# Performance work log

Hardware: AMD Instinct MI355X
Metric: run time of the kernel (lower is better)

## Reference

```python
import jax, jax.numpy as jnp
import numpy as np
from functools import partial

N = 10000      # nodes
E = 100000     # edges
WIDTH = 64     # node hidden width
KER_W = 1024   # kernel MLP hidden width
KER_IN = 6     # edge feature dim
DEPTH = 6


def setup_inputs() -> dict:
    key = jax.random.key(0)
    ks = jax.random.split(key, 16)

    def glorot(k, shape):
        fan_in = shape[0]
        return jax.random.normal(k, shape, dtype=jnp.float32) / np.sqrt(fan_in)

    inp = {
        "x": jax.random.normal(ks[0], (N, 1), dtype=jnp.float32),
        "edge_index": jax.random.randint(ks[1], (2, E), 0, N, dtype=jnp.int32),
        "edge_attr": jax.random.uniform(ks[2], (E, KER_IN), dtype=jnp.float32),
        # fc1: in_width=1 -> width
        "fc1_w": glorot(ks[3], (1, WIDTH)),
        "fc1_b": jnp.zeros((WIDTH,), jnp.float32),
        # kernel DenseNet: ker_in -> ker_width -> ker_width -> width**2 (ReLU between)
        "k1_w": glorot(ks[4], (KER_IN, KER_W)),
        "k1_b": jnp.zeros((KER_W,), jnp.float32),
        "k2_w": glorot(ks[5], (KER_W, KER_W)),
        "k2_b": jnp.zeros((KER_W,), jnp.float32),
        "k3_w": glorot(ks[6], (KER_W, WIDTH * WIDTH)),
        "k3_b": jnp.zeros((WIDTH * WIDTH,), jnp.float32),
        # NNConv_old root weight + bias
        "root_w": glorot(ks[7], (WIDTH, WIDTH)),
        "conv_b": jnp.zeros((WIDTH,), jnp.float32),
        # fc2: width -> 1
        "fc2_w": glorot(ks[8], (WIDTH, 1)),
        "fc2_b": jnp.zeros((1,), jnp.float32),
    }
    return inp


def reference(x, edge_index, edge_attr, fc1_w, fc1_b, k1_w, k1_b, k2_w, k2_b,
              k3_w, k3_b, root_w, conv_b, fc2_w, fc2_b):
    src = edge_index[0]  # x_j (source, gathered)
    dst = edge_index[1]  # aggregation target

    # Per-edge kernel MLP -> [E, width, width]. edge_attr is constant across
    # depth iterations, so compute the edge weights once (same math).
    h = jax.nn.relu(edge_attr @ k1_w + k1_b)
    h = jax.nn.relu(h @ k2_w + k2_b)
    ew = (h @ k3_w + k3_b).reshape(E, WIDTH, WIDTH)

    # mean aggregation denominators (scatter_mean semantics: deg clamped to 1)
    deg = jax.ops.segment_sum(jnp.ones((E,), jnp.float32), dst, num_segments=N)
    deg = jnp.maximum(deg, 1.0)[:, None]  # [N,1]

    z = x @ fc1_w + fc1_b  # [N, width]
    for _ in range(DEPTH):
        msg = jnp.einsum('ei,eio->eo', z[src], ew)            # gather + per-edge matmul
        agg = jax.ops.segment_sum(msg, dst, num_segments=N)   # scatter-add
        agg = agg / deg                                       # mean
        z = jax.nn.relu(agg + z @ root_w + conv_b)
    return z @ fc2_w + fc2_b  # [N, 1]
```

## Files before the change

kernel.cpp:

```cpp
#include <hip/hip_runtime.h>
#include <hip/hip_bf16.h>

#define N_NODES 10000
#define N_EDGES 100000
#define DEPTH   6
#define E_CHUNK 12500

typedef __attribute__((ext_vector_type(8))) short short8;
typedef __attribute__((ext_vector_type(4))) float f32x4;
typedef unsigned short u16;

__device__ __forceinline__ float bf2f(u16 u) {
    union { float f; unsigned int i; } v; v.i = ((unsigned int)u) << 16; return v.f;
}
__device__ __forceinline__ u16 f2bf(float f) {
    union { float f; unsigned int i; } v; v.f = f;
    unsigned int x = v.i;
    unsigned int r = (x + 0x7fffu + ((x >> 16) & 1u)) >> 16;
    return (u16)r;
}

__device__ __forceinline__ void gload_lds16(const void* g, void* s) {
    __builtin_amdgcn_global_load_lds((const __attribute__((address_space(1))) void*)g,
                                     (__attribute__((address_space(3))) void*)s, 16, 0, 0);
}

__global__ void k2_transpose_kernel(const float* __restrict__ k2w, u16* __restrict__ k2T) {
    int idx = blockIdx.x * 256 + threadIdx.x;
    int n = idx >> 10, k = idx & 1023;
    k2T[idx] = f2bf(k2w[k * 1024 + n]);
}
__global__ void k3_permT_kernel(const float* __restrict__ k3w, u16* __restrict__ k3pT) {
    int idx = blockIdx.x * 256 + threadIdx.x;
    int n = idx >> 10, c = idx & 1023;
    k3pT[idx] = f2bf(k3w[(size_t)c * 4096 + (n & 63) * 64 + (n >> 6)]);
}
__global__ void b3_permute_kernel(const float* __restrict__ b3, float* __restrict__ b3p) {
    int n = blockIdx.x * 256 + threadIdx.x;
    if (n >= 4096) return;
    b3p[n] = b3[(n & 63) * 64 + (n >> 6)];
}

__global__ void deg_kernel(const int* __restrict__ ei, float* __restrict__ deg) {
    int e = blockIdx.x * 256 + threadIdx.x;
    if (e < N_EDGES) atomicAdd(&deg[ei[N_EDGES + e]], 1.0f);
}

__global__ void gemm1_kernel(const float* __restrict__ ea, const float* __restrict__ k1w,
                             const float* __restrict__ k1b, u16* __restrict__ h1, int e0) {
    int idx = blockIdx.x * 256 + threadIdx.x;
    int c = idx & 1023;
    int e = (idx >> 10) + e0;
    float acc = k1b[c];
#pragma unroll
    for (int i = 0; i < 6; i++) acc += ea[e * 6 + i] * k1w[i * 1024 + c];
    h1[idx] = f2bf(fmaxf(acc, 0.0f));
}

template <int NOUT, bool RELU, bool FUSE_MSG>
__global__ __launch_bounds__(256) void gemm128_kernel(
    const u16* __restrict__ A, const u16* __restrict__ BT,
    const float* __restrict__ bias, u16* __restrict__ C, int M,
    const int* __restrict__ ei, const float* __restrict__ z,
    float* __restrict__ agg) {
    constexpr int K = 1024;
    __shared__ __align__(16) u16 Alds[128 * 32];
    __shared__ __align__(16) u16 Blds[128 * 32];

    const int t = threadIdx.x;
    const int lane = t & 63, w = t >> 6;
    const int wm = w >> 1, wn = w & 1;
    const int fm = lane & 15, q = lane >> 4;
    const int m0 = blockIdx.y * 128;
    const int n0 = blockIdx.x * 128;

    f32x4 acc[4][4];
#pragma unroll
    for (int a = 0; a < 4; a++)
#pragma unroll
        for (int b = 0; b < 4; b++) acc[a][b] = (f32x4){0.f, 0.f, 0.f, 0.f};

    int ar0 = m0 + (t >> 2);        if (ar0 >= M) ar0 = M - 1;
    int ar1 = m0 + 64 + (t >> 2);   if (ar1 >= M) ar1 = M - 1;
    const u16* gA0 = A + (size_t)ar0 * K + (t & 3) * 8;
    const u16* gA1 = A + (size_t)ar1 * K + (t & 3) * 8;
    const u16* gB0 = BT + (size_t)(n0 + (t >> 2)) * K + (t & 3) * 8;
    const u16* gB1 = BT + (size_t)(n0 + 64 + (t >> 2)) * K + (t & 3) * 8;
    u16* lA0 = &Alds[t * 8];
    u16* lA1 = &Alds[2048 + t * 8];
    u16* lB0 = &Blds[t * 8];
    u16* lB1 = &Blds[2048 + t * 8];

    for (int k0 = 0; k0 < K; k0 += 32) {
        gload_lds16(gA0 + k0, lA0);
        gload_lds16(gA1 + k0, lA1);
        gload_lds16(gB0 + k0, lB0);
        gload_lds16(gB1 + k0, lB1);
        __syncthreads();

        short8 af[4], bf[4];
#pragma unroll
        for (int mi = 0; mi < 4; mi++)
            af[mi] = *reinterpret_cast<const short8*>(&Alds[(wm * 64 + mi * 16 + fm) * 32 + q * 8]);
#pragma unroll
        for (int ni = 0; ni < 4; ni++)
            bf[ni] = *reinterpret_cast<const short8*>(&Blds[(wn * 64 + ni * 16 + fm) * 32 + q * 8]);
#pragma unroll
        for (int mi = 0; mi < 4; mi++)
#pragma unroll
            for (int ni = 0; ni < 4; ni++)
                acc[mi][ni] = __builtin_amdgcn_mfma_f32_16x16x32_bf16(af[mi], bf[ni], acc[mi][ni], 0, 0, 0);
        __syncthreads();
    }

    if (!FUSE_MSG) {
#pragma unroll
        for (int mi = 0; mi < 4; mi++) {
#pragma unroll
            for (int ni = 0; ni < 4; ni++) {
                int col = n0 + wn * 64 + ni * 16 + fm;
                float bsv = bias[col];
#pragma unroll
                for (int r = 0; r < 4; r++) {
                    int row = m0 + wm * 64 + mi * 16 + q * 4 + r;
                    if (row < M) {
                        float v = acc[mi][ni][r] + bsv;
                        if (RELU) v = fmaxf(v, 0.0f);
                        C[(size_t)row * NOUT + col] = f2bf(v);
                    }
                }
            }
        }
    } else {
        const int o = (n0 >> 6) + wn;
        float bsv[4];
        int iidx[4];
#pragma unroll
        for (int ni = 0; ni < 4; ni++) {
            bsv[ni] = bias[n0 + wn * 64 + ni * 16 + fm];
            iidx[ni] = ni * 16 + fm;
        }
#pragma unroll
        for (int mi = 0; mi < 4; mi++) {
#pragma unroll
            for (int r = 0; r < 4; r++) {
                int e = m0 + wm * 64 + mi * 16 + q * 4 + r;
                float partial = 0.f;
                int dst = 0;
                if (e < M) {
                    int src = ei[e];
                    dst = ei[N_EDGES + e];
                    const float* zs = z + (size_t)src * 64;
#pragma unroll
                    for (int ni = 0; ni < 4; ni++)
                        partial += (acc[mi][ni][r] + bsv[ni]) * zs[iidx[ni]];
                }
                partial += __shfl_xor(partial, 1);
                partial += __shfl_xor(partial, 2);
                partial += __shfl_xor(partial, 4);
                partial += __shfl_xor(partial, 8);
                if (fm == 0 && e < M) atomicAdd(&agg[(size_t)dst * 64 + o], partial);
            }
        }
    }
}

__global__ void z0_kernel(const float* __restrict__ x, const float* __restrict__ w,
                          const float* __restrict__ b, float* __restrict__ z) {
    int idx = blockIdx.x * 256 + threadIdx.x;
    int n = idx >> 6, o = idx & 63;
    z[idx] = x[n] * w[o] + b[o];
}

__global__ __launch_bounds__(256) void update_kernel(const float* __restrict__ zin,
                                                     const float* __restrict__ agg,
                                                     const float* __restrict__ deg,
                                                     const float* __restrict__ rootw,
                                                     const float* __restrict__ convb,
                                                     float* __restrict__ zout) {
    int n = blockIdx.x * 4 + (threadIdx.x >> 6);
    int o = threadIdx.x & 63;
    float r = convb[o];
    const float* zr = zin + (size_t)n * 64;
#pragma unroll 8
    for (int i = 0; i < 64; i++) r += zr[i] * rootw[i * 64 + o];
    float d = deg[n];
    d = d < 1.0f ? 1.0f : d;
    float v = agg[(size_t)n * 64 + o] / d + r;
    zout[(size_t)n * 64 + o] = fmaxf(v, 0.0f);
}

__global__ void final_kernel(const float* __restrict__ z, const float* __restrict__ w,
                             const float* __restrict__ b, float* __restrict__ out) {
    int n = blockIdx.x * 256 + threadIdx.x;
    if (n >= N_NODES) return;
    float acc = b[0];
#pragma unroll 8
    for (int o = 0; o < 64; o++) acc += z[(size_t)n * 64 + o] * w[o];
    out[n] = acc;
}

__global__ void dbg_kernel(float* __restrict__ out, float val, int n) {
    int i = blockIdx.x * 256 + threadIdx.x;
    if (i < n) out[i] = val;
}

extern "C" void kernel_launch(void* const* d_in, const int* in_sizes, int n_in,
                              void* d_out, int out_size, void* d_ws, size_t ws_size,
                              hipStream_t stream) {
    const float* x     = (const float*)d_in[0];
    const int*   ei    = (const int*)  d_in[1];
    const float* ea    = (const float*)d_in[2];
    const float* fc1w  = (const float*)d_in[3];
    const float* fc1b  = (const float*)d_in[4];
    const float* k1w   = (const float*)d_in[5];
    const float* k1b   = (const float*)d_in[6];
    const float* k2w   = (const float*)d_in[7];
    const float* k2b   = (const float*)d_in[8];
    const float* k3w   = (const float*)d_in[9];
    const float* k3b   = (const float*)d_in[10];
    const float* rootw = (const float*)d_in[11];
    const float* convb = (const float*)d_in[12];
    const float* fc2w  = (const float*)d_in[13];
    const float* fc2b  = (const float*)d_in[14];
    float* out = (float*)d_out;

    const size_t NEED = 249000000;
    if (ws_size < NEED) {
        dbg_kernel<<<(N_NODES + 255) / 256, 256, 0, stream>>>(out, (float)(ws_size >> 20), N_NODES);
        return;
    }

    char* p = (char*)d_ws;
    auto alloc = [&](size_t bytes) {
        char* r = p;
        p += (bytes + 255) & ~(size_t)255;
        return r;
    };
    u16*   h2   = (u16*)  alloc((size_t)N_EDGES * 1024 * 2);
    u16*   h1ch = (u16*)  alloc((size_t)E_CHUNK * 1024 * 2);
    u16*   k2T  = (u16*)  alloc((size_t)1024 * 1024 * 2);
    u16*   k3pT = (u16*)  alloc((size_t)4096 * 1024 * 2);
    float* b3p  = (float*)alloc(4096 * 4);
    float* zA   = (float*)alloc((size_t)N_NODES * 64 * 4);
    float* zB   = (float*)alloc((size_t)N_NODES * 64 * 4);
    float* agg  = (float*)alloc((size_t)N_NODES * 64 * 4);
    float* deg  = (float*)alloc((size_t)N_NODES * 4);

    hipMemsetAsync(deg, 0, (size_t)N_NODES * 4, stream);

    k2_transpose_kernel<<<(1024 * 1024) / 256, 256, 0, stream>>>(k2w, k2T);
    k3_permT_kernel<<<(4096 * 1024) / 256, 256, 0, stream>>>(k3w, k3pT);
    b3_permute_kernel<<<16, 256, 0, stream>>>(k3b, b3p);
    deg_kernel<<<(N_EDGES + 255) / 256, 256, 0, stream>>>(ei, deg);

    for (int e0 = 0; e0 < N_EDGES; e0 += E_CHUNK) {
        gemm1_kernel<<<(E_CHUNK * 1024) / 256, 256, 0, stream>>>(ea, k1w, k1b, h1ch, e0);
        dim3 g2(1024 / 128, (E_CHUNK + 127) / 128);
        gemm128_kernel<1024, true, false><<<g2, 256, 0, stream>>>(
            h1ch, k2T, k2b, h2 + (size_t)e0 * 1024, E_CHUNK, nullptr, nullptr, nullptr);
    }

    z0_kernel<<<(N_NODES * 64) / 256, 256, 0, stream>>>(x, fc1w, fc1b, zA);

    float* zin = zA;
    float* zout = zB;
    for (int d = 0; d < DEPTH; d++) {
        hipMemsetAsync(agg, 0, (size_t)N_NODES * 64 * 4, stream);
        dim3 g3(4096 / 128, (N_EDGES + 127) / 128);
        gemm128_kernel<4096, false, true><<<g3, 256, 0, stream>>>(
            h2, k3pT, b3p, nullptr, N_EDGES, ei, zin, agg);
        update_kernel<<<N_NODES / 4, 256, 0, stream>>>(zin, agg, deg, rootw, convb, zout);
        float* tmp = zin; zin = zout; zout = tmp;
    }

    final_kernel<<<(N_NODES + 255) / 256, 256, 0, stream>>>(zin, fc2w, fc2b, out);
}
```

Before: 7.586 ms.

## Replace fused k3 GEMM with 256x256 triple-buffered swizzled-LDS kernel

Adds a dedicated fused kernel for the per-depth k3 GEMM plus message-reduction. It uses 256x256 tiles with 512 threads, a three-stage LDS ring filled by global_load_lds with vmcnt-based waits, and an XOR swizzle on LDS columns to avoid bank conflicts. MFMA issue is interleaved with prefetch and wrapped in s_setprio. The larger tile is meant to raise arithmetic intensity and hide load latency in the dominant GEMM, at the cost of more registers and 96KB of LDS per block.

```diff
diff --git a/kernel.cpp b/kernel.cpp
--- a/kernel.cpp
+++ b/kernel.cpp
@@ -57,12 +57,10 @@
     h1[idx] = f2bf(fmaxf(acc, 0.0f));
 }
 
-template <int NOUT, bool RELU, bool FUSE_MSG>
+template <int NOUT, bool RELU>
 __global__ __launch_bounds__(256) void gemm128_kernel(
     const u16* __restrict__ A, const u16* __restrict__ BT,
-    const float* __restrict__ bias, u16* __restrict__ C, int M,
-    const int* __restrict__ ei, const float* __restrict__ z,
-    float* __restrict__ agg) {
+    const float* __restrict__ bias, u16* __restrict__ C, int M) {
     constexpr int K = 1024;
     __shared__ __align__(16) u16 Alds[128 * 32];
     __shared__ __align__(16) u16 Blds[128 * 32];
@@ -113,54 +111,155 @@
         __syncthreads();
     }
 
-    if (!FUSE_MSG) {
-#pragma unroll
-        for (int mi = 0; mi < 4; mi++) {
-#pragma unroll
-            for (int ni = 0; ni < 4; ni++) {
-                int col = n0 + wn * 64 + ni * 16 + fm;
-                float bsv = bias[col];
-#pragma unroll
-                for (int r = 0; r < 4; r++) {
-                    int row = m0 + wm * 64 + mi * 16 + q * 4 + r;
-                    if (row < M) {
-                        float v = acc[mi][ni][r] + bsv;
-                        if (RELU) v = fmaxf(v, 0.0f);
-                        C[(size_t)row * NOUT + col] = f2bf(v);
-                    }
+#pragma unroll
+    for (int mi = 0; mi < 4; mi++) {
+#pragma unroll
+        for (int ni = 0; ni < 4; ni++) {
+            int col = n0 + wn * 64 + ni * 16 + fm;
+            float bsv = bias[col];
+#pragma unroll
+            for (int r = 0; r < 4; r++) {
+                int row = m0 + wm * 64 + mi * 16 + q * 4 + r;
+                if (row < M) {
+                    float v = acc[mi][ni][r] + bsv;
+                    if (RELU) v = fmaxf(v, 0.0f);
+                    C[(size_t)row * NOUT + col] = f2bf(v);
                 }
             }
         }
-    } else {
-        const int o = (n0 >> 6) + wn;
-        float bsv[4];
-        int iidx[4];
-#pragma unroll
-        for (int ni = 0; ni < 4; ni++) {
-            bsv[ni] = bias[n0 + wn * 64 + ni * 16 + fm];
-            iidx[ni] = ni * 16 + fm;
-        }
-#pragma unroll
-        for (int mi = 0; mi < 4; mi++) {
-#pragma unroll
-            for (int r = 0; r < 4; r++) {
-                int e = m0 + wm * 64 + mi * 16 + q * 4 + r;
-                float partial = 0.f;
-                int dst = 0;
-                if (e < M) {
-                    int src = ei[e];
-                    dst = ei[N_EDGES + e];
-                    const float* zs = z + (size_t)src * 64;
-#pragma unroll
-                    for (int ni = 0; ni < 4; ni++)
-                        partial += (acc[mi][ni][r] + bsv[ni]) * zs[iidx[ni]];
-                }
-                partial += __shfl_xor(partial, 1);
-                partial += __shfl_xor(partial, 2);
-                partial += __shfl_xor(partial, 4);
-                partial += __shfl_xor(partial, 8);
-                if (fm == 0 && e < M) atomicAdd(&agg[(size_t)dst * 64 + o], partial);
+    }
+}
+
+__global__ __launch_bounds__(512, 2) void fused256_kernel(
+    const u16* __restrict__ A, const u16* __restrict__ BT,
+    const float* __restrict__ bias, const int* __restrict__ ei,
+    const float* __restrict__ z, float* __restrict__ agg) {
+    constexpr int KTILES = 32;
+    __shared__ __align__(16) u16 ldsA[3][256 * 32];
+    __shared__ __align__(16) u16 ldsB[3][256 * 32];
+
+    const int t = threadIdx.x;
+    const int lane = t & 63;
+    const int w = t >> 6;
+    const int wm = w >> 2, wn = w & 3;
+    const int fm = lane & 15, q = lane >> 4;
+    const int m0 = blockIdx.y * 256;
+    const int n0 = blockIdx.x * 256;
+
+    const u16* gA[2]; const u16* gB[2];
+    int dA[2], dB[2];
+#pragma unroll
+    for (int l = 0; l < 2; l++) {
+        int L = l * 512 + t;
+        int r = L >> 2;
+        int kq = (L & 3) ^ ((r >> 1) & 3);
+        int ra = m0 + r; if (ra >= N_EDGES) ra = N_EDGES - 1;
+        gA[l] = A + (size_t)ra * 1024 + kq * 8;
+        gB[l] = BT + (size_t)(n0 + r) * 1024 + kq * 8;
+        dA[l] = L * 8;
+        dB[l] = L * 8;
+    }
+    const int xq = q ^ ((fm >> 1) & 3);
+    const int aBase = (wm * 128 + fm) * 32 + xq * 8;
+    const int bBase = (wn * 64 + fm) * 32 + xq * 8;
+
+    f32x4 acc[8][4];
+#pragma unroll
+    for (int a = 0; a < 8; a++)
+#pragma unroll
+        for (int b = 0; b < 4; b++) acc[a][b] = (f32x4){0.f, 0.f, 0.f, 0.f};
+
+#pragma unroll
+    for (int tt = 0; tt < 2; tt++) {
+#pragma unroll
+        for (int l = 0; l < 2; l++) { gload_lds16(gA[l], &ldsA[tt][dA[l]]); gA[l] += 32; }
+#pragma unroll
+        for (int l = 0; l < 2; l++) { gload_lds16(gB[l], &ldsB[tt][dB[l]]); gB[l] += 32; }
+    }
+    asm volatile("s_waitcnt vmcnt(4)" ::: "memory");
+    __builtin_amdgcn_s_barrier();
+    asm volatile("" ::: "memory");
+
+    int cur = 0;
+    for (int kt = 0; kt < KTILES; ++kt) {
+        const bool stg = (kt + 2 < KTILES);
+        int nb = cur + 2; if (nb >= 3) nb -= 3;
+        const u16* la = ldsA[cur];
+        const u16* lb = ldsB[cur];
+
+        short8 bf[4], af[4];
+#pragma unroll
+        for (int ni = 0; ni < 4; ni++)
+            bf[ni] = *reinterpret_cast<const short8*>(&lb[bBase + ni * 512]);
+#pragma unroll
+        for (int mi = 0; mi < 4; mi++)
+            af[mi] = *reinterpret_cast<const short8*>(&la[aBase + mi * 512]);
+        if (stg) {
+#pragma unroll
+            for (int l = 0; l < 2; l++) { gload_lds16(gA[l], &ldsA[nb][dA[l]]); gA[l] += 32; }
+        }
+        __builtin_amdgcn_s_setprio(1);
+#pragma unroll
+        for (int mi = 0; mi < 4; mi++)
+#pragma unroll
+            for (int ni = 0; ni < 4; ni++)
+                acc[mi][ni] = __builtin_amdgcn_mfma_f32_16x16x32_bf16(af[mi], bf[ni], acc[mi][ni], 0, 0, 0);
+        __builtin_amdgcn_s_setprio(0);
+
+#pragma unroll
+        for (int mi = 0; mi < 4; mi++)
+            af[mi] = *reinterpret_cast<const short8*>(&la[aBase + 2048 + mi * 512]);
+        if (stg) {
+#pragma unroll
+            for (int l = 0; l < 2; l++) { gload_lds16(gB[l], &ldsB[nb][dB[l]]); gB[l] += 32; }
+        }
+        __builtin_amdgcn_s_setprio(1);
+#pragma unroll
+        for (int mi = 0; mi < 4; mi++)
+#pragma unroll
+            for (int ni = 0; ni < 4; ni++)
+                acc[4 + mi][ni] = __builtin_amdgcn_mfma_f32_16x16x32_bf16(af[mi], bf[ni], acc[4 + mi][ni], 0, 0, 0);
+        __builtin_amdgcn_s_setprio(0);
+
+        if (kt + 2 < KTILES) {
+            asm volatile("s_waitcnt vmcnt(4)" ::: "memory");
+        } else if (kt + 1 < KTILES) {
+            asm volatile("s_waitcnt vmcnt(0)" ::: "memory");
+        }
+        if (kt + 1 < KTILES) {
+            __builtin_amdgcn_s_barrier();
+            asm volatile("" ::: "memory");
+        }
+        cur = cur + 1; if (cur == 3) cur = 0;
+    }
+
+    const int o = (n0 >> 6) + wn;
+    float bsv[4]; int iidx[4];
+#pragma unroll
+    for (int ni = 0; ni < 4; ni++) {
+        bsv[ni] = bias[n0 + wn * 64 + ni * 16 + fm];
+        iidx[ni] = ni * 16 + fm;
+    }
+#pragma unroll
+    for (int mi = 0; mi < 8; mi++) {
+#pragma unroll
+        for (int r = 0; r < 4; r++) {
+            int e = m0 + wm * 128 + mi * 16 + q * 4 + r;
+            float partial = 0.f;
+            int dst = 0;
+            if (e < N_EDGES) {
+                int src = ei[e];
+                dst = ei[N_EDGES + e];
+                const float* zs = z + (size_t)src * 64;
+#pragma unroll
+                for (int ni = 0; ni < 4; ni++)
+                    partial += (acc[mi][ni][r] + bsv[ni]) * zs[iidx[ni]];
             }
+            partial += __shfl_xor(partial, 1);
+            partial += __shfl_xor(partial, 2);
+            partial += __shfl_xor(partial, 4);
+            partial += __shfl_xor(partial, 8);
+            if (fm == 0 && e < N_EDGES) atomicAdd(&agg[(size_t)dst * 64 + o], partial);
         }
     }
 }
@@ -257,8 +356,8 @@
     for (int e0 = 0; e0 < N_EDGES; e0 += E_CHUNK) {
         gemm1_kernel<<<(E_CHUNK * 1024) / 256, 256, 0, stream>>>(ea, k1w, k1b, h1ch, e0);
         dim3 g2(1024 / 128, (E_CHUNK + 127) / 128);
-        gemm128_kernel<1024, true, false><<<g2, 256, 0, stream>>>(
-            h1ch, k2T, k2b, h2 + (size_t)e0 * 1024, E_CHUNK, nullptr, nullptr, nullptr);
+        gemm128_kernel<1024, true><<<g2, 256, 0, stream>>>(
+            h1ch, k2T, k2b, h2 + (size_t)e0 * 1024, E_CHUNK);
     }
 
     z0_kernel<<<(N_NODES * 64) / 256, 256, 0, stream>>>(x, fc1w, fc1b, zA);
@@ -267,9 +366,8 @@
     float* zout = zB;
     for (int d = 0; d < DEPTH; d++) {
         hipMemsetAsync(agg, 0, (size_t)N_NODES * 64 * 4, stream);
-        dim3 g3(4096 / 128, (N_EDGES + 127) / 128);
-        gemm128_kernel<4096, false, true><<<g3, 256, 0, stream>>>(
-            h2, k3pT, b3p, nullptr, N_EDGES, ei, zin, agg);
+        dim3 g3(4096 / 256, (N_EDGES + 255) / 256);
+        fused256_kernel<<<g3, 512, 0, stream>>>(h2, k3pT, b3p, ei, zin, agg);
         update_kernel<<<N_NODES / 4, 256, 0, stream>>>(zin, agg, deg, rootw, convb, zout);
         float* tmp = zin; zin = zout; zout = tmp;
     }
```

After: 9.230 ms. +21.7%, slower.

## Triple-buffer LDS tiles with async prefetch and XOR swizzle in bf16 GEMM

Applied to the files above, without the earlier changes.

Replaces the single-buffered load-sync-compute loop in the 128x128 MFMA GEMM with a three-stage LDS ring. The next-but-one K tile is prefetched through global_load_lds while the current tile feeds the MFMAs, with explicit vmcnt waits and a single barrier per iteration. It also adds an XOR swizzle on the LDS k-quad index to reduce bank conflicts, and raises wave priority around the MFMA block. The aim is to hide global memory latency and remove one barrier per K step, at the cost of three times the LDS, which may lower occupancy.

```diff
diff --git a/kernel.cpp b/kernel.cpp
--- a/kernel.cpp
+++ b/kernel.cpp
@@ -64,8 +64,9 @@
     const int* __restrict__ ei, const float* __restrict__ z,
     float* __restrict__ agg) {
     constexpr int K = 1024;
-    __shared__ __align__(16) u16 Alds[128 * 32];
-    __shared__ __align__(16) u16 Blds[128 * 32];
+    constexpr int KTILES = 32;
+    __shared__ __align__(16) u16 ldsA[3][128 * 32];
+    __shared__ __align__(16) u16 ldsB[3][128 * 32];
 
     const int t = threadIdx.x;
     const int lane = t & 63, w = t >> 6;
@@ -80,37 +81,72 @@
 #pragma unroll
         for (int b = 0; b < 4; b++) acc[a][b] = (f32x4){0.f, 0.f, 0.f, 0.f};
 
-    int ar0 = m0 + (t >> 2);        if (ar0 >= M) ar0 = M - 1;
-    int ar1 = m0 + 64 + (t >> 2);   if (ar1 >= M) ar1 = M - 1;
-    const u16* gA0 = A + (size_t)ar0 * K + (t & 3) * 8;
-    const u16* gA1 = A + (size_t)ar1 * K + (t & 3) * 8;
-    const u16* gB0 = BT + (size_t)(n0 + (t >> 2)) * K + (t & 3) * 8;
-    const u16* gB1 = BT + (size_t)(n0 + 64 + (t >> 2)) * K + (t & 3) * 8;
-    u16* lA0 = &Alds[t * 8];
-    u16* lA1 = &Alds[2048 + t * 8];
-    u16* lB0 = &Blds[t * 8];
-    u16* lB1 = &Blds[2048 + t * 8];
-
-    for (int k0 = 0; k0 < K; k0 += 32) {
-        gload_lds16(gA0 + k0, lA0);
-        gload_lds16(gA1 + k0, lA1);
-        gload_lds16(gB0 + k0, lB0);
-        gload_lds16(gB1 + k0, lB1);
-        __syncthreads();
+    const u16* gA[2]; const u16* gB[2];
+    int dL[2];
+#pragma unroll
+    for (int l = 0; l < 2; l++) {
+        int L = l * 256 + t;
+        int r = L >> 2;
+        int kq = (L & 3) ^ ((r >> 1) & 3);
+        int ra = m0 + r; if (ra >= M) ra = M - 1;
+        gA[l] = A + (size_t)ra * K + kq * 8;
+        gB[l] = BT + (size_t)(n0 + r) * K + kq * 8;
+        dL[l] = L * 8;
+    }
+    const int xq = q ^ ((fm >> 1) & 3);
+    const int aB = (wm * 64 + fm) * 32 + xq * 8;
+    const int bB = (wn * 64 + fm) * 32 + xq * 8;
+
+#pragma unroll
+    for (int tt = 0; tt < 2; tt++) {
+#pragma unroll
+        for (int l = 0; l < 2; l++) { gload_lds16(gA[l], &ldsA[tt][dL[l]]); gA[l] += 32; }
+#pragma unroll
+        for (int l = 0; l < 2; l++) { gload_lds16(gB[l], &ldsB[tt][dL[l]]); gB[l] += 32; }
+    }
+    asm volatile("s_waitcnt vmcnt(4)" ::: "memory");
+    __builtin_amdgcn_s_barrier();
+    asm volatile("" ::: "memory");
+
+    int cur = 0;
+    for (int kt = 0; kt < KTILES; ++kt) {
+        const u16* la = ldsA[cur];
+        const u16* lb = ldsB[cur];
 
         short8 af[4], bf[4];
 #pragma unroll
         for (int mi = 0; mi < 4; mi++)
-            af[mi] = *reinterpret_cast<const short8*>(&Alds[(wm * 64 + mi * 16 + fm) * 32 + q * 8]);
+            af[mi] = *reinterpret_cast<const short8*>(&la[aB + mi * 512]);
 #pragma unroll
         for (int ni = 0; ni < 4; ni++)
-            bf[ni] = *reinterpret_cast<const short8*>(&Blds[(wn * 64 + ni * 16 + fm) * 32 + q * 8]);
+            bf[ni] = *reinterpret_cast<const short8*>(&lb[bB + ni * 512]);
+
+        if (kt + 2 < KTILES) {
+            int nb = cur + 2; if (nb >= 3) nb -= 3;
+#pragma unroll
+            for (int l = 0; l < 2; l++) { gload_lds16(gA[l], &ldsA[nb][dL[l]]); gA[l] += 32; }
+#pragma unroll
+            for (int l = 0; l < 2; l++) { gload_lds16(gB[l], &ldsB[nb][dL[l]]); gB[l] += 32; }
+        }
+
+        __builtin_amdgcn_s_setprio(1);
 #pragma unroll
         for (int mi = 0; mi < 4; mi++)
 #pragma unroll
             for (int ni = 0; ni < 4; ni++)
                 acc[mi][ni] = __builtin_amdgcn_mfma_f32_16x16x32_bf16(af[mi], bf[ni], acc[mi][ni], 0, 0, 0);
-        __syncthreads();
+        __builtin_amdgcn_s_setprio(0);
+
+        if (kt + 2 < KTILES) {
+            asm volatile("s_waitcnt vmcnt(4)" ::: "memory");
+        } else if (kt + 1 < KTILES) {
+            asm volatile("s_waitcnt vmcnt(0)" ::: "memory");
+        }
+        if (kt + 1 < KTILES) {
+            __builtin_amdgcn_s_barrier();
+            asm volatile("" ::: "memory");
+        }
+        cur = cur + 1; if (cur == 3) cur = 0;
     }
 
     if (!FUSE_MSG) {
```

Measured after the change: 7.496 ms, median of 3. About the same (-1.2%).
